# Kernel optimization log

Hardware: AMD Instinct MI355X
Metric: run time of the kernel (lower is better)

Reference implementation:

```python
import jax, jax.numpy as jnp
import numpy as np

B = 8            # batch
P = 28           # patch grid (224 / 8 for wide_resnet50_2 layer2)
D = 1536         # 512 (layer2) + 1024 (layer3) channels
M = 50000        # memory bank size
NUM_NEIGHBORS = 9
INPUT_SIZE = 224
SIGMA = 4.0
KSIZE = 2 * int(4.0 * SIGMA + 0.5) + 1  # 33, anomalib GaussianBlur2d convention


def setup_inputs() -> dict:
    key = jax.random.key(0)
    k1, k2 = jax.random.split(key)
    embedding = jax.random.normal(k1, (B * P * P, D), dtype=jnp.float32)
    memory_bank = jax.random.normal(k2, (M, D), dtype=jnp.float32)
    return {"embedding": embedding, "memory_bank": memory_bank}


def euclidean_dist(x, y):
    x_norm = jnp.sum(x * x, axis=-1, keepdims=True)
    y_norm = jnp.sum(y * y, axis=-1, keepdims=True)
    res = x_norm - 2.0 * jnp.matmul(x, jnp.swapaxes(y, -2, -1)) + jnp.swapaxes(y_norm, -2, -1)
    return jnp.sqrt(jnp.clip(res, 0.0, None))


def gaussian_kernel1d(ksize, sigma):
    x = jnp.arange(ksize, dtype=jnp.float32) - (ksize - 1) / 2.0
    g = jnp.exp(-(x * x) / (2.0 * sigma * sigma))
    return g / jnp.sum(g)


def gaussian_blur(img):
    # separable depthwise gaussian blur with reflect padding (kornia/anomalib style), img: [B,1,H,W]
    g = gaussian_kernel1d(KSIZE, SIGMA)
    pad = KSIZE // 2
    img = jnp.pad(img, ((0, 0), (0, 0), (pad, pad), (pad, pad)), mode='reflect')
    kh = g.reshape(1, 1, KSIZE, 1)
    kw = g.reshape(1, 1, 1, KSIZE)
    dn = ('NCHW', 'OIHW', 'NCHW')
    img = jax.lax.conv_general_dilated(img, kh, (1, 1), 'VALID', dimension_numbers=dn)
    img = jax.lax.conv_general_dilated(img, kw, (1, 1), 'VALID', dimension_numbers=dn)
    return img


def reference(embedding, memory_bank):
    # ---- nearest_neighbors(embedding, n_neighbors=1) ----
    dists = euclidean_dist(embedding, memory_bank)            # [B*P*P, M]
    patch_scores = jnp.min(dists, axis=1).reshape(B, P * P)   # [B, P*P]
    locations = jnp.argmin(dists, axis=1).reshape(B, P * P)   # [B, P*P]

    # ---- compute_anomaly_score (num_neighbors = 9) ----
    batch_idx = jnp.arange(B)
    max_patches = jnp.argmax(patch_scores, axis=1)                       # [B]
    feats = embedding.reshape(B, P * P, D)
    max_patches_features = feats[batch_idx, max_patches]                 # [B, D]
    score = patch_scores[batch_idx, max_patches]                         # [B]
    nn_index = locations[batch_idx, max_patches]                         # [B]
    nn_sample = memory_bank[nn_index]                                    # [B, D]
    d2 = euclidean_dist(nn_sample, memory_bank)                          # [B, M]
    _, support_samples = jax.lax.top_k(-d2, NUM_NEIGHBORS)               # smallest-k, ascending
    supp_feats = memory_bank[support_samples]                            # [B, K, D]
    d3 = euclidean_dist(max_patches_features[:, None, :], supp_feats)    # [B, 1, K]
    weights = (1.0 - jax.nn.softmax(d3[:, 0, :], axis=1))[:, 0]          # [B]
    pred_score = weights * score                                         # [B]

    # ---- anomaly map: bilinear upsample (align_corners=False) + gaussian blur ----
    pmap = patch_scores.reshape(B, 1, P, P)
    amap = jax.image.resize(pmap, (B, 1, INPUT_SIZE, INPUT_SIZE), method='bilinear')
    anomaly_map = gaussian_blur(amap)                                    # [B,1,224,224]
    return anomaly_map, pred_score
```

## Files before the change

kernel.cpp:

```cpp
#include <hip/hip_runtime.h>
#include <cstdint>
#include <cstddef>

#define DDIM 1536
#define NROWS 6272
#define NROWPAD 6400
#define MBANK 50000
#define NCOLPAD 50176
#define NRT 25
#define NCT 196
#define NCT4 (NCT * 4)
#define NKT8 12
#define NB 8
#define PP 784
#define HW 224
#define KS 33
#define PAD 16

typedef __attribute__((ext_vector_type(4))) int int4v;
typedef __attribute__((ext_vector_type(4))) float floatx4;

__device__ __forceinline__ unsigned long long u64min(unsigned long long a, unsigned long long b) {
  return a < b ? a : b;
}

__global__ __launch_bounds__(256) void convnorm8_kernel(const float* __restrict__ in,
                                                        signed char* __restrict__ out,
                                                        float* __restrict__ norm,
                                                        int valid_rows, int total_rows) {
  int row = blockIdx.x * 4 + (threadIdx.x >> 6);
  int lane = threadIdx.x & 63;
  if (row >= total_rows) return;
  int* dst = (int*)(out + (size_t)row * DDIM);
  float s = 0.f;
  if (row < valid_rows) {
    const float4* src = (const float4*)(in + (size_t)row * DDIM);
#pragma unroll
    for (int i = 0; i < 6; i++) {
      int d = lane + i * 64;
      float4 v = src[d];
      s = fmaf(v.x, v.x, s); s = fmaf(v.y, v.y, s);
      s = fmaf(v.z, v.z, s); s = fmaf(v.w, v.w, s);
      int q0 = min(max((int)rintf(v.x * 16.f), -127), 127);
      int q1 = min(max((int)rintf(v.y * 16.f), -127), 127);
      int q2 = min(max((int)rintf(v.z * 16.f), -127), 127);
      int q3 = min(max((int)rintf(v.w * 16.f), -127), 127);
      dst[d] = (q0 & 255) | ((q1 & 255) << 8) | ((q2 & 255) << 16) | ((q3 & 255) << 24);
    }
  } else {
#pragma unroll
    for (int i = 0; i < 6; i++) dst[lane + i * 64] = 0;
  }
  for (int off = 32; off; off >>= 1) s += __shfl_down(s, off, 64);
  if (lane == 0) norm[row] = s;
}

__global__ __launch_bounds__(256) void rownorm_kernel(const float* __restrict__ x,
                                                      float* __restrict__ out, int rows) {
  int row = blockIdx.x;
  if (row >= rows) return;
  const float4* p4 = (const float4*)(x + (size_t)row * DDIM);
  float s = 0.f;
  for (int d = threadIdx.x; d < DDIM / 4; d += 256) {
    float4 v = p4[d];
    s = fmaf(v.x, v.x, s); s = fmaf(v.y, v.y, s);
    s = fmaf(v.z, v.z, s); s = fmaf(v.w, v.w, s);
  }
  for (int off = 32; off; off >>= 1) s += __shfl_down(s, off, 64);
  __shared__ float ls[4];
  int wid = threadIdx.x >> 6, lane = threadIdx.x & 63;
  if (lane == 0) ls[wid] = s;
  __syncthreads();
  if (threadIdx.x == 0) out[row] = ls[0] + ls[1] + ls[2] + ls[3];
}

__global__ void init_u64_kernel(unsigned long long* p, int n) {
  int i = blockIdx.x * 256 + threadIdx.x;
  if (i < n) p[i] = ~0ull;
}

__global__ __launch_bounds__(512, 2) void mindist_mfma_kernel(
    const signed char* __restrict__ Ah, const signed char* __restrict__ Bh,
    const float* __restrict__ xnorm, const float* __restrict__ ynorm,
    unsigned long long* __restrict__ cand) {
  __shared__ char smem[131072];

  const int t = threadIdx.x;
  const int lane = t & 63, wid = t >> 6;
  const int wm = wid >> 2, wn = wid & 3;
  const int l15 = lane & 15, g = lane >> 4;

  const int nwg = NRT * NCT;
  const int q8 = nwg >> 3, r8 = nwg & 7;
  int orig = blockIdx.x;
  int xcd = orig & 7, pos = orig >> 3;
  int wg = (xcd < r8 ? xcd * (q8 + 1) : r8 * (q8 + 1) + (xcd - r8) * q8) + pos;
  const int rt = wg / NCT, ct = wg % NCT;
  const int row0 = rt * 256;
  const int c0 = ct * 256;

  const int ck0 = ((0 + g) ^ (l15 & 7)) << 4;
  const int ck1 = ((4 + g) ^ (l15 & 7)) << 4;
  const int aB = wm * 16384 + l15 * 128;
  const int bB = 65536 + (wn * 64 + l15) * 128;

  const int cl = (t & 7) ^ ((t >> 3) & 7);
  const signed char* paBase = Ah + (size_t)(row0 + (t >> 3)) * DDIM + cl * 16;
  const signed char* pbBase = Bh + (size_t)(c0 + (t >> 3)) * DDIM + cl * 16;

#define STAGE_KT(kt, d)                                                                  \
  {                                                                                      \
    _Pragma("unroll") for (int j = 0; j < 4; j++) {                                      \
      __builtin_amdgcn_global_load_lds(                                                  \
          (const __attribute__((address_space(1))) void*)(paBase +                       \
              (size_t)(j * 64) * DDIM + (size_t)(kt) * 128),                             \
          (__attribute__((address_space(3))) void*)(smem + (d) * 32768 + j * 8192 +      \
                                                    wid * 1024),                         \
          16, 0, 0);                                                                     \
    }                                                                                    \
    _Pragma("unroll") for (int j = 0; j < 4; j++) {                                      \
      __builtin_amdgcn_global_load_lds(                                                  \
          (const __attribute__((address_space(1))) void*)(pbBase +                       \
              (size_t)(j * 64) * DDIM + (size_t)(kt) * 128),                             \
          (__attribute__((address_space(3))) void*)(smem + 65536 + (d) * 32768 +         \
                                                    j * 8192 + wid * 1024),              \
          16, 0, 0);                                                                     \
    }                                                                                    \
  }

  int4v acc[8][4];
  int4v zz = {0, 0, 0, 0};
#pragma unroll
  for (int mi = 0; mi < 8; mi++)
#pragma unroll
    for (int nf = 0; nf < 4; nf++) acc[mi][nf] = zz;

  STAGE_KT(0, 0);
  STAGE_KT(1, 1);

  int4v ra[4][2], rbL[2][2], rbH[2][2];

  for (int kt = 0; kt < NKT8; ++kt) {
    const int d = kt & 1;
    if (kt < NKT8 - 1) {
      asm volatile("s_waitcnt vmcnt(8)" ::: "memory");
    } else {
      asm volatile("s_waitcnt vmcnt(0)" ::: "memory");
    }
    __builtin_amdgcn_sched_barrier(0);
    __builtin_amdgcn_s_barrier();
    __builtin_amdgcn_sched_barrier(0);

    const char* sA = smem + d * 32768 + aB;
    const char* sB = smem + d * 32768 + bB;

#pragma unroll
    for (int mi = 0; mi < 4; mi++) {
      ra[mi][0] = *(const int4v*)(sA + mi * 2048 + ck0);
      ra[mi][1] = *(const int4v*)(sA + mi * 2048 + ck1);
    }
#pragma unroll
    for (int nf = 0; nf < 2; nf++) {
      rbL[nf][0] = *(const int4v*)(sB + nf * 2048 + ck0);
      rbL[nf][1] = *(const int4v*)(sB + nf * 2048 + ck1);
    }
    asm volatile("s_waitcnt lgkmcnt(0)" ::: "memory");
    __builtin_amdgcn_sched_barrier(0);
    __builtin_amdgcn_s_setprio(1);
#pragma unroll
    for (int mi = 0; mi < 4; mi++)
#pragma unroll
      for (int nf = 0; nf < 2; nf++)
#pragma unroll
        for (int ks = 0; ks < 2; ks++)
          acc[mi][nf] = __builtin_amdgcn_mfma_i32_16x16x64_i8(ra[mi][ks], rbL[nf][ks],
                                                              acc[mi][nf], 0, 0, 0);
    __builtin_amdgcn_s_setprio(0);
    __builtin_amdgcn_sched_barrier(0);
    __builtin_amdgcn_s_barrier();
    __builtin_amdgcn_sched_barrier(0);

#pragma unroll
    for (int nf = 0; nf < 2; nf++) {
      rbH[nf][0] = *(const int4v*)(sB + (nf + 2) * 2048 + ck0);
      rbH[nf][1] = *(const int4v*)(sB + (nf + 2) * 2048 + ck1);
    }
    asm volatile("s_waitcnt lgkmcnt(0)" ::: "memory");
    __builtin_amdgcn_sched_barrier(0);
    __builtin_amdgcn_s_setprio(1);
#pragma unroll
    for (int mi = 0; mi < 4; mi++)
#pragma unroll
      for (int nf = 0; nf < 2; nf++)
#pragma unroll
        for (int ks = 0; ks < 2; ks++)
          acc[mi][nf + 2] = __builtin_amdgcn_mfma_i32_16x16x64_i8(
              ra[mi][ks], rbH[nf][ks], acc[mi][nf + 2], 0, 0, 0);
    __builtin_amdgcn_s_setprio(0);
    __builtin_amdgcn_sched_barrier(0);
    __builtin_amdgcn_s_barrier();
    __builtin_amdgcn_sched_barrier(0);

#pragma unroll
    for (int mi = 0; mi < 4; mi++) {
      ra[mi][0] = *(const int4v*)(sA + (mi + 4) * 2048 + ck0);
      ra[mi][1] = *(const int4v*)(sA + (mi + 4) * 2048 + ck1);
    }
    asm volatile("s_waitcnt lgkmcnt(0)" ::: "memory");
    __builtin_amdgcn_sched_barrier(0);
    __builtin_amdgcn_s_setprio(1);
#pragma unroll
    for (int mi = 0; mi < 4; mi++)
#pragma unroll
      for (int nf = 0; nf < 2; nf++)
#pragma unroll
        for (int ks = 0; ks < 2; ks++)
          acc[mi + 4][nf + 2] = __builtin_amdgcn_mfma_i32_16x16x64_i8(
              ra[mi][ks], rbH[nf][ks], acc[mi + 4][nf + 2], 0, 0, 0);
    __builtin_amdgcn_s_setprio(0);
    __builtin_amdgcn_sched_barrier(0);
    __builtin_amdgcn_s_barrier();
    __builtin_amdgcn_sched_barrier(0);

    if (kt < NKT8 - 2) STAGE_KT(kt + 2, d);
    __builtin_amdgcn_s_setprio(1);
#pragma unroll
    for (int mi = 0; mi < 4; mi++)
#pragma unroll
      for (int nf = 0; nf < 2; nf++)
#pragma unroll
        for (int ks = 0; ks < 2; ks++)
          acc[mi + 4][nf] = __builtin_amdgcn_mfma_i32_16x16x64_i8(
              ra[mi][ks], rbL[nf][ks], acc[mi + 4][nf], 0, 0, 0);
    __builtin_amdgcn_s_setprio(0);
  }
#undef STAGE_KT

  float yn[4];
  int colv[4];
#pragma unroll
  for (int nf = 0; nf < 4; nf++) {
    int col = c0 + wn * 64 + nf * 16 + l15;
    colv[nf] = col;
    yn[nf] = (col < MBANK) ? ynorm[col] : 0.f;
  }
#pragma unroll
  for (int mi = 0; mi < 8; mi++) {
    int rowb = row0 + wm * 128 + mi * 16 + g * 4;
#pragma unroll
    for (int q = 0; q < 4; q++) {
      float xnq = xnorm[rowb + q];
      unsigned long long best = ~0ull;
#pragma unroll
      for (int nf = 0; nf < 4; nf++) {
        if (colv[nf] < MBANK) {
          float dsq = fmaxf(xnq + yn[nf] - (float)acc[mi][nf][q] * 0.0078125f, 0.f);
          unsigned long long pk =
              ((unsigned long long)__float_as_uint(dsq) << 32) | (unsigned)colv[nf];
          best = u64min(best, pk);
        }
      }
#pragma unroll
      for (int mask = 1; mask <= 8; mask <<= 1)
        best = u64min(best, __shfl_xor(best, mask, 64));
      if (l15 == 0 && rowb + q < NROWS)
        cand[(size_t)(rowb + q) * NCT4 + ct * 4 + wn] = best;
    }
  }
}

__global__ __launch_bounds__(256) void rerank_kernel(
    const float* __restrict__ emb, const float* __restrict__ mem,
    const float* __restrict__ xnorm, const float* __restrict__ ynorm,
    const unsigned long long* __restrict__ cand, float* __restrict__ ps,
    int* __restrict__ loc) {
  int row = blockIdx.x, t = threadIdx.x;
  int lane = t & 63, wave = t >> 6;
  __shared__ unsigned long long lred[4];
  __shared__ int glist[64];
  __shared__ int gcount;
  __shared__ float gmin;
  const unsigned long long* crow = cand + (size_t)row * NCT4;
  unsigned long long mn = ~0ull;
  for (int i = t; i < NCT4; i += 256) mn = u64min(mn, crow[i]);
  for (int off = 32; off; off >>= 1) {
    unsigned long long o = __shfl_down(mn, off, 64);
    mn = u64min(mn, o);
  }
  if (lane == 0) lred[wave] = mn;
  if (t == 0) gcount = 0;
  __syncthreads();
  if (t == 0) {
    unsigned long long m0 = lred[0];
    for (int w = 1; w < 4; w++) m0 = u64min(m0, lred[w]);
    gmin = __uint_as_float((unsigned)(m0 >> 32));
  }
  __syncthreads();
  float gate = gmin + 14.0f;
  for (int i = t; i < NCT4; i += 256) {
    unsigned long long v = crow[i];
    float dq = __uint_as_float((unsigned)(v >> 32));
    if (dq <= gate) {
      int idx = atomicAdd(&gcount, 1);
      if (idx < 64) glist[idx] = (int)(v & 0xffffffffu);
    }
  }
  __syncthreads();
  int ng = min(gcount, 64);
  float xnv = xnorm[row];
  const float4* xp = (const float4*)(emb + (size_t)row * DDIM);
  unsigned long long best = ~0ull;
  for (int gi = wave; gi < ng; gi += 4) {
    int col = glist[gi];
    const float4* yp = (const float4*)(mem + (size_t)col * DDIM);
    float s = 0.f;
    for (int d4 = lane; d4 < DDIM / 4; d4 += 64) {
      float4 a = xp[d4], b = yp[d4];
      s = fmaf(a.x, b.x, s); s = fmaf(a.y, b.y, s);
      s = fmaf(a.z, b.z, s); s = fmaf(a.w, b.w, s);
    }
    for (int off = 32; off; off >>= 1) s += __shfl_down(s, off, 64);
    if (lane == 0) {
      float dsq = fmaxf(xnv + ynorm[col] - 2.f * s, 0.f);
      unsigned long long pk =
          ((unsigned long long)__float_as_uint(dsq) << 32) | (unsigned)col;
      best = u64min(best, pk);
    }
  }
  if (lane == 0) lred[wave] = best;
  __syncthreads();
  if (t == 0) {
    unsigned long long b = lred[0];
    for (int w = 1; w < 4; w++) b = u64min(b, lred[w]);
    ps[row] = sqrtf(__uint_as_float((unsigned)(b >> 32)));
    loc[row] = (int)(b & 0xffffffffu);
  }
}

#define BM 128
#define BN 128
#define DKC 16
#define FCSPLIT 16
#define FCT ((MBANK + BN - 1) / BN)
#define FCPB ((FCT + FCSPLIT - 1) / FCSPLIT)

__global__ __launch_bounds__(256) void mindist_kernel(
    const float* __restrict__ A, const float* __restrict__ Bm,
    const float* __restrict__ xnorm, const float* __restrict__ ynorm,
    unsigned long long* __restrict__ best) {
  __shared__ float Asf[DKC][BM];
  __shared__ float Bsf[DKC][BN];
  int t = threadIdx.x;
  int tx = t & 15, ty = t >> 4;
  int row0 = blockIdx.x * BM;
  int rloc[8], cloc[8];
#pragma unroll
  for (int i = 0; i < 4; i++) {
    rloc[i] = ty * 4 + i; rloc[i + 4] = 64 + ty * 4 + i;
    cloc[i] = tx * 4 + i; cloc[i + 4] = 64 + tx * 4 + i;
  }
  float xnv[8];
#pragma unroll
  for (int i = 0; i < 8; i++) xnv[i] = xnorm[row0 + rloc[i]];
  unsigned long long bestr[8];
#pragma unroll
  for (int i = 0; i < 8; i++) bestr[i] = ~0ull;
  int ct_begin = blockIdx.y * FCPB;
  int ct_end = ct_begin + FCPB; if (ct_end > FCT) ct_end = FCT;
  for (int ct = ct_begin; ct < ct_end; ++ct) {
    int c0 = ct * BN;
    float acc[8][8];
#pragma unroll
    for (int i = 0; i < 8; i++)
#pragma unroll
      for (int j = 0; j < 8; j++) acc[i][j] = 0.f;
    for (int dk = 0; dk < DDIM; dk += DKC) {
#pragma unroll
      for (int s = 0; s < 2; ++s) {
        int q = t + s * 256;
        int r = q >> 2, c4 = q & 3;
        float4 va = *(const float4*)(A + (size_t)(row0 + r) * DDIM + dk + c4 * 4);
        Asf[c4 * 4 + 0][r] = va.x; Asf[c4 * 4 + 1][r] = va.y;
        Asf[c4 * 4 + 2][r] = va.z; Asf[c4 * 4 + 3][r] = va.w;
        int col = c0 + r;
        float4 vb = make_float4(0.f, 0.f, 0.f, 0.f);
        if (col < MBANK) vb = *(const float4*)(Bm + (size_t)col * DDIM + dk + c4 * 4);
        Bsf[c4 * 4 + 0][r] = vb.x; Bsf[c4 * 4 + 1][r] = vb.y;
        Bsf[c4 * 4 + 2][r] = vb.z; Bsf[c4 * 4 + 3][r] = vb.w;
      }
      __syncthreads();
#pragma unroll
      for (int k = 0; k < DKC; k++) {
        float4 a0 = *(const float4*)&Asf[k][ty * 4];
        float4 a1 = *(const float4*)&Asf[k][64 + ty * 4];
        float4 b0 = *(const float4*)&Bsf[k][tx * 4];
        float4 b1 = *(const float4*)&Bsf[k][64 + tx * 4];
        float av[8] = {a0.x, a0.y, a0.z, a0.w, a1.x, a1.y, a1.z, a1.w};
        float bv[8] = {b0.x, b0.y, b0.z, b0.w, b1.x, b1.y, b1.z, b1.w};
#pragma unroll
        for (int i = 0; i < 8; i++)
#pragma unroll
          for (int j = 0; j < 8; j++) acc[i][j] = fmaf(av[i], bv[j], acc[i][j]);
      }
      __syncthreads();
    }
#pragma unroll
    for (int j = 0; j < 8; j++) {
      int col = c0 + cloc[j];
      if (col < MBANK) {
        float yn = ynorm[col];
#pragma unroll
        for (int i = 0; i < 8; i++) {
          float dsq = fmaxf(xnv[i] + yn - 2.f * acc[i][j], 0.f);
          unsigned long long pk =
              ((unsigned long long)__float_as_uint(dsq) << 32) | (unsigned)col;
          if (pk < bestr[i]) bestr[i] = pk;
        }
      }
    }
  }
#pragma unroll
  for (int i = 0; i < 8; i++) atomicMin(&best[row0 + rloc[i]], bestr[i]);
}

__global__ void unpack_kernel(const unsigned long long* __restrict__ best,
                              float* __restrict__ ps, int* __restrict__ loc) {
  int i = blockIdx.x * 256 + threadIdx.x;
  if (i >= NROWS) return;
  unsigned long long v = best[i];
  ps[i] = sqrtf(__uint_as_float((unsigned)(v >> 32)));
  loc[i] = (int)(v & 0xffffffffu);
}

__global__ __launch_bounds__(256) void argmax_kernel(const float* __restrict__ ps,
                                                     const int* __restrict__ loc,
                                                     float* __restrict__ bscore,
                                                     int* __restrict__ bfrow,
                                                     int* __restrict__ bnn) {
  int b = blockIdx.x, t = threadIdx.x;
  unsigned long long bp = 0;
  for (int p = t; p < PP; p += 256) {
    unsigned long long pk = ((unsigned long long)__float_as_uint(ps[b * PP + p]) << 32) |
                            (unsigned)(0xffffffffu - (unsigned)p);
    if (pk > bp) bp = pk;
  }
  for (int off = 32; off; off >>= 1) {
    unsigned long long o = __shfl_down(bp, off, 64);
    if (o > bp) bp = o;
  }
  __shared__ unsigned long long ls[4];
  int wid = t >> 6, lane = t & 63;
  if (lane == 0) ls[wid] = bp;
  __syncthreads();
  if (t == 0) {
    for (int w = 1; w < 4; w++) if (ls[w] > ls[0]) ls[0] = ls[w];
    unsigned p = 0xffffffffu - (unsigned)(ls[0] & 0xffffffffu);
    bscore[b] = __uint_as_float((unsigned)(ls[0] >> 32));
    bfrow[b] = b * PP + (int)p;
    bnn[b] = loc[b * PP + (int)p];
  }
}

__global__ __launch_bounds__(256) void d2_kernel(const float* __restrict__ mem,
                                                 const float* __restrict__ ynorm,
                                                 const int* __restrict__ bnn,
                                                 float* __restrict__ d2) {
  __shared__ float nn8[NB][DDIM];
  __shared__ float nnorm[NB];
  for (int e = threadIdx.x; e < NB * DDIM; e += 256) {
    int b = e / DDIM, d = e % DDIM;
    nn8[b][d] = mem[(size_t)bnn[b] * DDIM + d];
  }
  if (threadIdx.x < NB) nnorm[threadIdx.x] = ynorm[bnn[threadIdx.x]];
  __syncthreads();
  int wid = threadIdx.x >> 6, lane = threadIdx.x & 63;
  int gw = blockIdx.x * 4 + wid;
  int nw = gridDim.x * 4;
  for (int m = gw; m < MBANK; m += nw) {
    const float4* mp4 = (const float4*)(mem + (size_t)m * DDIM);
    float acc[NB];
#pragma unroll
    for (int b = 0; b < NB; b++) acc[b] = 0.f;
    for (int d4 = lane; d4 < DDIM / 4; d4 += 64) {
      float4 v = mp4[d4];
#pragma unroll
      for (int b = 0; b < NB; b++) {
        float4 w = *(const float4*)&nn8[b][d4 * 4];
        acc[b] = fmaf(v.x, w.x, acc[b]); acc[b] = fmaf(v.y, w.y, acc[b]);
        acc[b] = fmaf(v.z, w.z, acc[b]); acc[b] = fmaf(v.w, w.w, acc[b]);
      }
    }
    float yn = ynorm[m];
#pragma unroll
    for (int b = 0; b < NB; b++) {
      float r = acc[b];
      for (int off = 32; off; off >>= 1) r += __shfl_down(r, off, 64);
      if (lane == 0) d2[(size_t)b * MBANK + m] = sqrtf(fmaxf(nnorm[b] + yn - 2.f * r, 0.f));
    }
  }
}

__global__ __launch_bounds__(256) void topk_kernel(
    const float* __restrict__ emb, const float* __restrict__ mem,
    const float* __restrict__ xnorm, const float* __restrict__ ynorm,
    const float* __restrict__ d2, const float* __restrict__ bscore,
    const int* __restrict__ bfrow, float* __restrict__ pred) {
  int b = blockIdx.x, t = threadIdx.x;
  __shared__ unsigned long long ls9[256][9];
  __shared__ float fred[4];
  __shared__ int supp[9];
  __shared__ float d3s[9];
  const float* row = d2 + (size_t)b * MBANK;
  unsigned long long a0 = ~0ull, a1 = ~0ull, a2 = ~0ull, a3 = ~0ull, a4 = ~0ull,
                     a5 = ~0ull, a6 = ~0ull, a7 = ~0ull, a8 = ~0ull;
  for (int m = t; m < MBANK; m += 256) {
    unsigned long long pk = ((unsigned long long)__float_as_uint(row[m]) << 32) | (unsigned)m;
    if (pk < a8) {
      a8 = pk;
      unsigned long long tv;
#define CSWP(x, y) if (y < x) { tv = x; x = y; y = tv; }
      CSWP(a7, a8) CSWP(a6, a7) CSWP(a5, a6) CSWP(a4, a5)
      CSWP(a3, a4) CSWP(a2, a3) CSWP(a1, a2) CSWP(a0, a1)
#undef CSWP
    }
  }
  ls9[t][0] = a0; ls9[t][1] = a1; ls9[t][2] = a2; ls9[t][3] = a3; ls9[t][4] = a4;
  ls9[t][5] = a5; ls9[t][6] = a6; ls9[t][7] = a7; ls9[t][8] = a8;
  __syncthreads();
  for (int s = 128; s >= 1; s >>= 1) {
    if (t < s) {
      unsigned long long outv[9];
      int i = 0, j = 0;
#pragma unroll
      for (int k = 0; k < 9; k++) {
        unsigned long long x = ls9[t][i], y = ls9[t + s][j];
        if (x <= y) { outv[k] = x; i++; } else { outv[k] = y; j++; }
      }
#pragma unroll
      for (int k = 0; k < 9; k++) ls9[t][k] = outv[k];
    }
    __syncthreads();
  }
  if (t < 9) supp[t] = (int)(ls9[0][t] & 0xffffffffu);
  __syncthreads();
  int frow = bfrow[b];
  const float* x = emb + (size_t)frow * DDIM;
  float xnv = xnorm[frow];
  for (int k = 0; k < 9; k++) {
    const float* y = mem + (size_t)supp[k] * DDIM;
    float s = 0.f;
    for (int d = t; d < DDIM; d += 256) s = fmaf(x[d], y[d], s);
    for (int off = 32; off; off >>= 1) s += __shfl_down(s, off, 64);
    if ((t & 63) == 0) fred[t >> 6] = s;
    __syncthreads();
    if (t == 0) {
      float dot = fred[0] + fred[1] + fred[2] + fred[3];
      d3s[k] = sqrtf(fmaxf(xnv - 2.f * dot + ynorm[supp[k]], 0.f));
    }
    __syncthreads();
  }
  if (t == 0) {
    float mx = d3s[0];
    for (int k = 1; k < 9; k++) mx = fmaxf(mx, d3s[k]);
    float sum = 0.f;
    for (int k = 0; k < 9; k++) sum += expf(d3s[k] - mx);
    float w = 1.f - expf(d3s[0] - mx) / sum;
    pred[b] = w * bscore[b];
  }
}

__global__ void gauss_kernel(float* __restrict__ g) {
  __shared__ float tmp[KS];
  int t = threadIdx.x;
  if (t < KS) {
    float x = (float)t - (float)(KS - 1) * 0.5f;
    tmp[t] = __expf(-(x * x) / 32.0f);
  }
  __syncthreads();
  if (t == 0) {
    float s = 0.f;
    for (int j = 0; j < KS; j++) s += tmp[j];
    for (int j = 0; j < KS; j++) g[j] = tmp[j] / s;
  }
}

__global__ __launch_bounds__(256) void resize_kernel(const float* __restrict__ ps,
                                                     float* __restrict__ out) {
  int idx = blockIdx.x * 256 + threadIdx.x;
  if (idx >= NB * HW * HW) return;
  int x = idx % HW, y = (idx / HW) % HW, b = idx / (HW * HW);
  float sx = (x + 0.5f) * 0.125f - 0.5f;
  float sy = (y + 0.5f) * 0.125f - 0.5f;
  int x0 = (int)floorf(sx), y0 = (int)floorf(sy);
  float fx = sx - x0, fy = sy - y0;
  int x0c = min(max(x0, 0), 27), x1c = min(max(x0 + 1, 0), 27);
  int y0c = min(max(y0, 0), 27), y1c = min(max(y0 + 1, 0), 27);
  const float* p = ps + b * PP;
  float v00 = p[y0c * 28 + x0c], v01 = p[y0c * 28 + x1c];
  float v10 = p[y1c * 28 + x0c], v11 = p[y1c * 28 + x1c];
  out[idx] = v00 * (1.f - fy) * (1.f - fx) + v01 * (1.f - fy) * fx +
             v10 * fy * (1.f - fx) + v11 * fy * fx;
}

__device__ __forceinline__ int reflect224(int i) {
  if (i < 0) i = -i;
  if (i > 223) i = 446 - i;
  return i;
}

__global__ __launch_bounds__(256) void blurv_kernel(const float* __restrict__ in,
                                                    const float* __restrict__ g,
                                                    float* __restrict__ out) {
  __shared__ float gk[KS];
  if (threadIdx.x < KS) gk[threadIdx.x] = g[threadIdx.x];
  __syncthreads();
  int idx = blockIdx.x * 256 + threadIdx.x;
  if (idx >= NB * HW * HW) return;
  int x = idx % HW, y = (idx / HW) % HW, b = idx / (HW * HW);
  const float* base = in + (size_t)b * HW * HW;
  float s = 0.f;
#pragma unroll
  for (int j = 0; j < KS; j++) {
    int yy = reflect224(y - PAD + j);
    s = fmaf(gk[j], base[yy * HW + x], s);
  }
  out[idx] = s;
}

__global__ __launch_bounds__(256) void blurh_kernel(const float* __restrict__ in,
                                                    const float* __restrict__ g,
                                                    float* __restrict__ out) {
  __shared__ float gk[KS];
  if (threadIdx.x < KS) gk[threadIdx.x] = g[threadIdx.x];
  __syncthreads();
  int idx = blockIdx.x * 256 + threadIdx.x;
  if (idx >= NB * HW * HW) return;
  int x = idx % HW, y = (idx / HW) % HW, b = idx / (HW * HW);
  const float* base = in + (size_t)b * HW * HW;
  float s = 0.f;
#pragma unroll
  for (int j = 0; j < KS; j++) {
    int xx = reflect224(x - PAD + j);
    s = fmaf(gk[j], base[y * HW + xx], s);
  }
  out[idx] = s;
}

extern "C" void kernel_launch(void* const* d_in, const int* in_sizes, int n_in,
                              void* d_out, int out_size, void* d_ws, size_t ws_size,
                              hipStream_t stream) {
  const float* emb = (const float*)d_in[0];
  const float* mem = (const float*)d_in[1];
  float* out = (float*)d_out;

  char* ws = (char*)d_ws;
  size_t off = 0;
  auto alloc = [&](size_t bytes) -> void* {
    void* p = ws + off;
    off += (bytes + 255) & ~(size_t)255;
    return p;
  };
  float* ynorm = (float*)alloc((size_t)NCOLPAD * 4);
  float* xnorm = (float*)alloc((size_t)NROWPAD * 4);
  unsigned long long* cand =
      (unsigned long long*)alloc((size_t)NROWS * NCT4 * 8);
  float* ps = (float*)alloc(NROWS * 4);
  int* loc = (int*)alloc(NROWS * 4);
  float* bscore = (float*)alloc(NB * 4);
  int* bfrow = (int*)alloc(NB * 4);
  int* bnn = (int*)alloc(NB * 4);
  float* d2 = (float*)alloc((size_t)NB * MBANK * 4);
  float* g = (float*)alloc(KS * 4);
  float* rsz = (float*)alloc((size_t)NB * HW * HW * 4);
  float* tmp = (float*)alloc((size_t)NB * HW * HW * 4);
  signed char* emb_q = (signed char*)alloc((size_t)NROWPAD * DDIM);
  signed char* mem_q = (signed char*)alloc((size_t)NCOLPAD * DDIM);
  size_t full_need = off;

  bool fast = (ws_size >= full_need);

  if (fast) {
    convnorm8_kernel<<<NCOLPAD / 4, 256, 0, stream>>>(mem, mem_q, ynorm, MBANK, NCOLPAD);
    convnorm8_kernel<<<NROWPAD / 4, 256, 0, stream>>>(emb, emb_q, xnorm, NROWS, NROWPAD);
    mindist_mfma_kernel<<<NRT * NCT, 512, 0, stream>>>(emb_q, mem_q, xnorm, ynorm, cand);
    rerank_kernel<<<NROWS, 256, 0, stream>>>(emb, mem, xnorm, ynorm, cand, ps, loc);
    argmax_kernel<<<NB, 256, 0, stream>>>(ps, loc, bscore, bfrow, bnn);
  } else {
    rownorm_kernel<<<MBANK, 256, 0, stream>>>(mem, ynorm, MBANK);
    rownorm_kernel<<<NROWS, 256, 0, stream>>>(emb, xnorm, NROWS);
    unsigned long long* best = cand;
    init_u64_kernel<<<(NROWS + 255) / 256, 256, 0, stream>>>(best, NROWS);
    mindist_kernel<<<dim3(NROWS / BM, FCSPLIT), 256, 0, stream>>>(emb, mem, xnorm, ynorm,
                                                                  best);
    unpack_kernel<<<(NROWS + 255) / 256, 256, 0, stream>>>(best, ps, loc);
    argmax_kernel<<<NB, 256, 0, stream>>>(ps, loc, bscore, bfrow, bnn);
  }

  d2_kernel<<<1200, 256, 0, stream>>>(mem, ynorm, bnn, d2);
  topk_kernel<<<NB, 256, 0, stream>>>(emb, mem, xnorm, ynorm, d2, bscore, bfrow,
                                      out + (size_t)NB * HW * HW);
  gauss_kernel<<<1, 64, 0, stream>>>(g);
  resize_kernel<<<(NB * HW * HW + 255) / 256, 256, 0, stream>>>(ps, rsz);
  blurv_kernel<<<(NB * HW * HW + 255) / 256, 256, 0, stream>>>(rsz, g, tmp);
  blurh_kernel<<<(NB * HW * HW + 255) / 256, 256, 0, stream>>>(tmp, g, out);
}
```

Measured before the change: 1.085 ms.

## Shrink int8 MFMA distance tile to 128x128 with 256-thread workgroups

The int8 MFMA min-distance GEMM goes from 256x256 tiles with 8 waves to 128x128 tiles with 4 waves. This halves LDS use and the accumulator registers, which should let more workgroups run per CU. The three-phase interleaved MFMA schedule and its explicit LDS waits become one load-then-compute phase per k-step. The workgroup-to-XCD mapping is simplified and the candidate buffer now holds two slots per column tile. In exchange, each loaded byte is reused half as often, so global and L2 traffic roughly doubles, and the rerank pass must scan more candidate slots.

```diff
diff --git a/kernel.cpp b/kernel.cpp
--- a/kernel.cpp
+++ b/kernel.cpp
@@ -7,9 +7,9 @@
 #define NROWPAD 6400
 #define MBANK 50000
 #define NCOLPAD 50176
-#define NRT 25
-#define NCT 196
-#define NCT4 (NCT * 4)
+#define NRT 49
+#define NCT 392
+#define NSLOT (NCT * 2)
 #define NKT8 12
 #define NB 8
 #define PP 784
@@ -79,30 +79,27 @@
   if (i < n) p[i] = ~0ull;
 }
 
-__global__ __launch_bounds__(512, 2) void mindist_mfma_kernel(
+__global__ __launch_bounds__(256, 2) void mindist_mfma_kernel(
     const signed char* __restrict__ Ah, const signed char* __restrict__ Bh,
     const float* __restrict__ xnorm, const float* __restrict__ ynorm,
     unsigned long long* __restrict__ cand) {
-  __shared__ char smem[131072];
+  __shared__ char smem[65536];
 
   const int t = threadIdx.x;
   const int lane = t & 63, wid = t >> 6;
-  const int wm = wid >> 2, wn = wid & 3;
+  const int wm = wid >> 1, wn = wid & 1;
   const int l15 = lane & 15, g = lane >> 4;
 
-  const int nwg = NRT * NCT;
-  const int q8 = nwg >> 3, r8 = nwg & 7;
-  int orig = blockIdx.x;
-  int xcd = orig & 7, pos = orig >> 3;
-  int wg = (xcd < r8 ? xcd * (q8 + 1) : r8 * (q8 + 1) + (xcd - r8) * q8) + pos;
-  const int rt = wg / NCT, ct = wg % NCT;
-  const int row0 = rt * 256;
-  const int c0 = ct * 256;
+  const int xcd = blockIdx.x & 7, pos = blockIdx.x >> 3;
+  const int ct = xcd * 49 + pos / 49;
+  const int rt = pos % 49;
+  const int row0 = rt * 128;
+  const int c0 = ct * 128;
 
   const int ck0 = ((0 + g) ^ (l15 & 7)) << 4;
   const int ck1 = ((4 + g) ^ (l15 & 7)) << 4;
-  const int aB = wm * 16384 + l15 * 128;
-  const int bB = 65536 + (wn * 64 + l15) * 128;
+  const int aBase = wm * 8192 + l15 * 128;
+  const int bBase = 32768 + wn * 8192 + l15 * 128;
 
   const int cl = (t & 7) ^ ((t >> 3) & 7);
   const signed char* paBase = Ah + (size_t)(row0 + (t >> 3)) * DDIM + cl * 16;
@@ -113,32 +110,30 @@
     _Pragma("unroll") for (int j = 0; j < 4; j++) {                                      \
       __builtin_amdgcn_global_load_lds(                                                  \
           (const __attribute__((address_space(1))) void*)(paBase +                       \
-              (size_t)(j * 64) * DDIM + (size_t)(kt) * 128),                             \
-          (__attribute__((address_space(3))) void*)(smem + (d) * 32768 + j * 8192 +      \
+              (size_t)(j * 32) * DDIM + (size_t)(kt) * 128),                             \
+          (__attribute__((address_space(3))) void*)(smem + (d) * 16384 + j * 4096 +      \
                                                     wid * 1024),                         \
           16, 0, 0);                                                                     \
     }                                                                                    \
     _Pragma("unroll") for (int j = 0; j < 4; j++) {                                      \
       __builtin_amdgcn_global_load_lds(                                                  \
           (const __attribute__((address_space(1))) void*)(pbBase +                       \
-              (size_t)(j * 64) * DDIM + (size_t)(kt) * 128),                             \
-          (__attribute__((address_space(3))) void*)(smem + 65536 + (d) * 32768 +         \
-                                                    j * 8192 + wid * 1024),              \
+              (size_t)(j * 32) * DDIM + (size_t)(kt) * 128),                             \
+          (__attribute__((address_space(3))) void*)(smem + 32768 + (d) * 16384 +         \
+                                                    j * 4096 + wid * 1024),              \
           16, 0, 0);                                                                     \
     }                                                                                    \
   }
 
-  int4v acc[8][4];
+  int4v acc[4][4];
   int4v zz = {0, 0, 0, 0};
 #pragma unroll
-  for (int mi = 0; mi < 8; mi++)
+  for (int mi = 0; mi < 4; mi++)
 #pragma unroll
     for (int nf = 0; nf < 4; nf++) acc[mi][nf] = zz;
 
   STAGE_KT(0, 0);
   STAGE_KT(1, 1);
-
-  int4v ra[4][2], rbL[2][2], rbH[2][2];
 
   for (int kt = 0; kt < NKT8; ++kt) {
     const int d = kt & 1;
@@ -151,88 +146,34 @@
     __builtin_amdgcn_s_barrier();
     __builtin_amdgcn_sched_barrier(0);
 
-    const char* sA = smem + d * 32768 + aB;
-    const char* sB = smem + d * 32768 + bB;
-
+    const char* sA = smem + d * 16384 + aBase;
+    const char* sB = smem + d * 16384 + bBase;
+
+    int4v ra[4][2], rb[4][2];
 #pragma unroll
     for (int mi = 0; mi < 4; mi++) {
       ra[mi][0] = *(const int4v*)(sA + mi * 2048 + ck0);
       ra[mi][1] = *(const int4v*)(sA + mi * 2048 + ck1);
     }
 #pragma unroll
-    for (int nf = 0; nf < 2; nf++) {
-      rbL[nf][0] = *(const int4v*)(sB + nf * 2048 + ck0);
-      rbL[nf][1] = *(const int4v*)(sB + nf * 2048 + ck1);
-    }
-    asm volatile("s_waitcnt lgkmcnt(0)" ::: "memory");
-    __builtin_amdgcn_sched_barrier(0);
+    for (int nf = 0; nf < 4; nf++) {
+      rb[nf][0] = *(const int4v*)(sB + nf * 2048 + ck0);
+      rb[nf][1] = *(const int4v*)(sB + nf * 2048 + ck1);
+    }
     __builtin_amdgcn_s_setprio(1);
 #pragma unroll
     for (int mi = 0; mi < 4; mi++)
 #pragma unroll
-      for (int nf = 0; nf < 2; nf++)
+      for (int nf = 0; nf < 4; nf++)
 #pragma unroll
         for (int ks = 0; ks < 2; ks++)
-          acc[mi][nf] = __builtin_amdgcn_mfma_i32_16x16x64_i8(ra[mi][ks], rbL[nf][ks],
+          acc[mi][nf] = __builtin_amdgcn_mfma_i32_16x16x64_i8(ra[mi][ks], rb[nf][ks],
                                                               acc[mi][nf], 0, 0, 0);
     __builtin_amdgcn_s_setprio(0);
     __builtin_amdgcn_sched_barrier(0);
     __builtin_amdgcn_s_barrier();
     __builtin_amdgcn_sched_barrier(0);
-
-#pragma unroll
-    for (int nf = 0; nf < 2; nf++) {
-      rbH[nf][0] = *(const int4v*)(sB + (nf + 2) * 2048 + ck0);
-      rbH[nf][1] = *(const int4v*)(sB + (nf + 2) * 2048 + ck1);
-    }
-    asm volatile("s_waitcnt lgkmcnt(0)" ::: "memory");
-    __builtin_amdgcn_sched_barrier(0);
-    __builtin_amdgcn_s_setprio(1);
-#pragma unroll
-    for (int mi = 0; mi < 4; mi++)
-#pragma unroll
-      for (int nf = 0; nf < 2; nf++)
-#pragma unroll
-        for (int ks = 0; ks < 2; ks++)
-          acc[mi][nf + 2] = __builtin_amdgcn_mfma_i32_16x16x64_i8(
-              ra[mi][ks], rbH[nf][ks], acc[mi][nf + 2], 0, 0, 0);
-    __builtin_amdgcn_s_setprio(0);
-    __builtin_amdgcn_sched_barrier(0);
-    __builtin_amdgcn_s_barrier();
-    __builtin_amdgcn_sched_barrier(0);
-
-#pragma unroll
-    for (int mi = 0; mi < 4; mi++) {
-      ra[mi][0] = *(const int4v*)(sA + (mi + 4) * 2048 + ck0);
-      ra[mi][1] = *(const int4v*)(sA + (mi + 4) * 2048 + ck1);
-    }
-    asm volatile("s_waitcnt lgkmcnt(0)" ::: "memory");
-    __builtin_amdgcn_sched_barrier(0);
-    __builtin_amdgcn_s_setprio(1);
-#pragma unroll
-    for (int mi = 0; mi < 4; mi++)
-#pragma unroll
-      for (int nf = 0; nf < 2; nf++)
-#pragma unroll
-        for (int ks = 0; ks < 2; ks++)
-          acc[mi + 4][nf + 2] = __builtin_amdgcn_mfma_i32_16x16x64_i8(
-              ra[mi][ks], rbH[nf][ks], acc[mi + 4][nf + 2], 0, 0, 0);
-    __builtin_amdgcn_s_setprio(0);
-    __builtin_amdgcn_sched_barrier(0);
-    __builtin_amdgcn_s_barrier();
-    __builtin_amdgcn_sched_barrier(0);
-
     if (kt < NKT8 - 2) STAGE_KT(kt + 2, d);
-    __builtin_amdgcn_s_setprio(1);
-#pragma unroll
-    for (int mi = 0; mi < 4; mi++)
-#pragma unroll
-      for (int nf = 0; nf < 2; nf++)
-#pragma unroll
-        for (int ks = 0; ks < 2; ks++)
-          acc[mi + 4][nf] = __builtin_amdgcn_mfma_i32_16x16x64_i8(
-              ra[mi][ks], rbL[nf][ks], acc[mi + 4][nf], 0, 0, 0);
-    __builtin_amdgcn_s_setprio(0);
   }
 #undef STAGE_KT
 
@@ -245,8 +186,8 @@
     yn[nf] = (col < MBANK) ? ynorm[col] : 0.f;
   }
 #pragma unroll
-  for (int mi = 0; mi < 8; mi++) {
-    int rowb = row0 + wm * 128 + mi * 16 + g * 4;
+  for (int mi = 0; mi < 4; mi++) {
+    int rowb = row0 + wm * 64 + mi * 16 + g * 4;
 #pragma unroll
     for (int q = 0; q < 4; q++) {
       float xnq = xnorm[rowb + q];
@@ -264,7 +205,7 @@
       for (int mask = 1; mask <= 8; mask <<= 1)
         best = u64min(best, __shfl_xor(best, mask, 64));
       if (l15 == 0 && rowb + q < NROWS)
-        cand[(size_t)(rowb + q) * NCT4 + ct * 4 + wn] = best;
+        cand[(size_t)(rowb + q) * NSLOT + ct * 2 + wn] = best;
     }
   }
 }
@@ -280,9 +221,9 @@
   __shared__ int glist[64];
   __shared__ int gcount;
   __shared__ float gmin;
-  const unsigned long long* crow = cand + (size_t)row * NCT4;
+  const unsigned long long* crow = cand + (size_t)row * NSLOT;
   unsigned long long mn = ~0ull;
-  for (int i = t; i < NCT4; i += 256) mn = u64min(mn, crow[i]);
+  for (int i = t; i < NSLOT; i += 256) mn = u64min(mn, crow[i]);
   for (int off = 32; off; off >>= 1) {
     unsigned long long o = __shfl_down(mn, off, 64);
     mn = u64min(mn, o);
@@ -297,7 +238,7 @@
   }
   __syncthreads();
   float gate = gmin + 14.0f;
-  for (int i = t; i < NCT4; i += 256) {
+  for (int i = t; i < NSLOT; i += 256) {
     unsigned long long v = crow[i];
     float dq = __uint_as_float((unsigned)(v >> 32));
     if (dq <= gate) {
@@ -663,7 +604,7 @@
   float* ynorm = (float*)alloc((size_t)NCOLPAD * 4);
   float* xnorm = (float*)alloc((size_t)NROWPAD * 4);
   unsigned long long* cand =
-      (unsigned long long*)alloc((size_t)NROWS * NCT4 * 8);
+      (unsigned long long*)alloc((size_t)NROWS * NSLOT * 8);
   float* ps = (float*)alloc(NROWS * 4);
   int* loc = (int*)alloc(NROWS * 4);
   float* bscore = (float*)alloc(NB * 4);
@@ -682,7 +623,7 @@
   if (fast) {
     convnorm8_kernel<<<NCOLPAD / 4, 256, 0, stream>>>(mem, mem_q, ynorm, MBANK, NCOLPAD);
     convnorm8_kernel<<<NROWPAD / 4, 256, 0, stream>>>(emb, emb_q, xnorm, NROWS, NROWPAD);
-    mindist_mfma_kernel<<<NRT * NCT, 512, 0, stream>>>(emb_q, mem_q, xnorm, ynorm, cand);
+    mindist_mfma_kernel<<<NRT * NCT, 256, 0, stream>>>(emb_q, mem_q, xnorm, ynorm, cand);
     rerank_kernel<<<NROWS, 256, 0, stream>>>(emb, mem, xnorm, ynorm, cand, ps, loc);
     argmax_kernel<<<NB, 256, 0, stream>>>(ps, loc, bscore, bfrow, bnn);
   } else {
```

Result: no change. 1.089 ms (+0.4%).
